# Optimization experiments

Hardware: AMD Instinct MI355X
Metric: run time of the kernel (lower is better)

## Reference

```python
import jax, jax.numpy as jnp
import numpy as np


def _conv(x, w, b, stride, pad):
    # NCHW conv, OIHW weights, bias add
    y = jax.lax.conv_general_dilated(
        x, w, (stride, stride), [(pad, pad), (pad, pad)],
        dimension_numbers=('NCHW', 'OIHW', 'NCHW'))
    return y + b[None, :, None, None]


def setup_inputs() -> dict:
    key = jax.random.key(0)
    ks = jax.random.split(key, 8)
    s = 0.05  # small init so SiLU chains stay numerically tame
    f32 = jnp.float32
    return {
        'x': jax.random.normal(ks[0], (8, 3, 640, 640), f32),
        'w0': jax.random.normal(ks[1], (32, 3, 3, 3), f32) * s,
        'b0': jnp.zeros((32,), f32),
        'w1': jax.random.normal(ks[2], (64, 32, 3, 3), f32) * s,
        'b1': jnp.zeros((64,), f32),
        'wc0': jax.random.normal(ks[3], (64, 64, 1, 1), f32) * s,
        'bc0': jnp.zeros((64,), f32),
        'wb1': jax.random.normal(ks[4], (32, 32, 3, 3), f32) * s,
        'bb1': jnp.zeros((32,), f32),
        'wb2': jax.random.normal(ks[5], (32, 32, 3, 3), f32) * s,
        'bb2': jnp.zeros((32,), f32),
        'wc1': jax.random.normal(ks[6], (64, 96, 1, 1), f32) * s,
        'bc1': jnp.zeros((64,), f32),
        'w3': jax.random.normal(ks[7], (128, 64, 3, 3), f32) * s,
        'b3': jnp.zeros((128,), f32),
    }


def reference(x, w0, b0, w1, b1, wc0, bc0, wb1, bb1, wb2, bb2, wc1, bc1, w3, b3):
    silu = jax.nn.silu
    # stem: conv0 (s2) + conv1 (s2), each Conv+SiLU
    h = silu(_conv(x, w0, b0, 2, 1))     # [B,32,320,320]
    h = silu(_conv(h, w1, b1, 2, 1))     # [B,64,160,160]
    # C2f block: 1x1 conv, split channels in half, residual bottleneck, concat, 1x1 conv
    y = silu(_conv(h, wc0, bc0, 1, 0))   # [B,64,160,160]
    x1, x2 = jnp.split(y, 2, axis=1)     # each [B,32,160,160]
    b = silu(_conv(x2, wb1, bb1, 1, 1))
    b = silu(_conv(b, wb2, bb2, 1, 1))
    b = x2 + b                           # shortcut=True bottleneck
    cat = jnp.concatenate([x1, x2, b], axis=1)  # [B,96,160,160] == 192*w
    h = silu(_conv(cat, wc1, bc1, 1, 0))  # [B,64,160,160]
    # conv3: downsample stage (s2)
    out = silu(_conv(h, w3, b3, 2, 1))    # [B,128,80,80]
    return out
```

## Files before the change

### kernel.cpp

```cpp
#include <hip/hip_runtime.h>
#include <hip/hip_bf16.h>

typedef __attribute__((ext_vector_type(8))) short short8;
typedef __attribute__((ext_vector_type(16))) float f32x16;
typedef __attribute__((ext_vector_type(4))) float f32x4;
typedef __attribute__((ext_vector_type(4))) unsigned int uint4v;
typedef __attribute__((ext_vector_type(4))) unsigned short ushort4v;

__device__ __forceinline__ float silu_f(float v) {
    return v * __builtin_amdgcn_rcpf(1.0f + __expf(-v));
}
__device__ __forceinline__ unsigned short bfhi(float v) {
    __hip_bfloat16 h = __float2bfloat16(v);
    return *reinterpret_cast<unsigned short*>(&h);
}
__device__ __forceinline__ float bf2f(unsigned short u) {
    __hip_bfloat16 h;
    *reinterpret_cast<unsigned short*>(&h) = u;
    return __bfloat162float(h);
}

__global__ __launch_bounds__(256) void prep_small(
    const float* __restrict__ w1, const float* __restrict__ wc0,
    const float* __restrict__ wb1, const float* __restrict__ wb2,
    const float* __restrict__ wc1, const float* __restrict__ w0,
    unsigned short* __restrict__ arena)
{
    const int u = blockIdx.x * 256 + threadIdx.x;
    if (u >= 6016) return;
    const int lane = u & 63, pf = u >> 6;
    float wv[8];
    if (pf < 36) {
        const int q = pf, cc = q & 1, rnd = (q >> 1) & 1, tap = q >> 2;
        const int co = cc * 32 + (lane & 31), ci0 = rnd * 16 + (lane >> 5) * 8;
        #pragma unroll
        for (int j = 0; j < 8; ++j) wv[j] = w1[(co * 32 + ci0 + j) * 9 + tap];
    } else if (pf < 44) {
        const int q = pf - 36, cc = q & 1, rnd = q >> 1;
        const int co = cc * 32 + (lane & 31), ci0 = rnd * 16 + (lane >> 5) * 8;
        #pragma unroll
        for (int j = 0; j < 8; ++j) wv[j] = wc0[co * 64 + ci0 + j];
    } else if (pf < 62) {
        const int q = pf - 44, rnd = q & 1, tap = q >> 1;
        const int co = lane & 31, ci0 = rnd * 16 + (lane >> 5) * 8;
        #pragma unroll
        for (int j = 0; j < 8; ++j) wv[j] = wb1[(co * 32 + ci0 + j) * 9 + tap];
    } else if (pf < 80) {
        const int q = pf - 62, rnd = q & 1, tap = q >> 1;
        const int co = lane & 31, ci0 = rnd * 16 + (lane >> 5) * 8;
        #pragma unroll
        for (int j = 0; j < 8; ++j) wv[j] = wb2[(co * 32 + ci0 + j) * 9 + tap];
    } else if (pf < 92) {
        const int q = pf - 80, cc = q & 1, rnd = q >> 1;
        const int co = cc * 32 + (lane & 31), ci0 = rnd * 16 + (lane >> 5) * 8;
        #pragma unroll
        for (int j = 0; j < 8; ++j) wv[j] = wc1[co * 96 + ci0 + j];
    } else {
        const int co = lane & 31;
        const int k0 = (pf - 92) * 16 + (lane >> 5) * 8;
        #pragma unroll
        for (int j = 0; j < 8; ++j) {
            const int k = k0 + j;
            wv[j] = (k < 27) ? w0[(co * 3 + k / 9) * 9 + (k % 9)] : 0.0f;
        }
    }
    unsigned short hs[8], ls[8];
    #pragma unroll
    for (int j = 0; j < 8; ++j) {
        unsigned short hh = bfhi(wv[j]);
        hs[j] = hh; ls[j] = bfhi(wv[j] - bf2f(hh));
    }
    *reinterpret_cast<short8*>(&arena[pf * 1024 + lane * 8])       = *(short8*)hs;
    *reinterpret_cast<short8*>(&arena[pf * 1024 + 512 + lane * 8]) = *(short8*)ls;
}

__global__ __launch_bounds__(256) void prep_w3(
    const float* __restrict__ w3, unsigned short* __restrict__ arena)
{
    const int u = blockIdx.x * 256 + threadIdx.x;
    const int lane = u & 63, pf = u >> 6;
    const int cc = pf & 1, rr = (pf >> 1) & 3, t9 = pf >> 3;
    const int tap = t9 % 9, cg = t9 / 9;
    const int co = cg * 64 + cc * 32 + (lane & 31);
    const int ci0 = rr * 16 + (lane >> 5) * 8;
    unsigned short hs[8], ls[8];
    #pragma unroll
    for (int j = 0; j < 8; ++j) {
        float wv = w3[(co * 64 + ci0 + j) * 9 + tap];
        unsigned short hh = bfhi(wv);
        hs[j] = hh; ls[j] = bfhi(wv - bf2f(hh));
    }
    *reinterpret_cast<short8*>(&arena[pf * 1024 + lane * 8])       = *(short8*)hs;
    *reinterpret_cast<short8*>(&arena[pf * 1024 + 512 + lane * 8]) = *(short8*)ls;
}

__global__ __launch_bounds__(256, 4) void stem_fused(
    const float* __restrict__ x, const unsigned short* __restrict__ wfr,
    const unsigned short* __restrict__ wc0fr, const float* __restrict__ b0,
    const float* __restrict__ bias, const float* __restrict__ bc0,
    unsigned short* __restrict__ ycl)
{
    __shared__ unsigned short lds[20800];
    const int tid = threadIdx.x;
    const int wv = tid >> 6, lane = tid & 63;
    const int p = lane & 31, h = lane >> 5;
    const int r = wv >> 1, cc = wv & 1;
    const int bx = blockIdx.x % 5, by = blockIdx.x / 5;
    const int ox0 = bx * 32, oy0 = by * 2;
    const int n = blockIdx.z;
    const float* xb = x + (long)n * 1228800;

    const int h8 = h * 8;
    int doff[16];
    #pragma unroll
    for (int idx = 0; idx < 16; ++idx) {
        const int k = (idx >> 3) * 16 + h8 + (idx & 7);
        if (k < 27) {
            const int ci = (k * 57) >> 9;
            const int tap = k - 9 * ci;
            const int dy = (tap * 11) >> 5, dx = tap - 3 * dy;
            doff[idx] = ci * 409600 + (dy - 1) * 640 + (dx - 1);
        } else {
            doff[idx] = 0;
        }
    }

    for (int it = 0; it < 3; ++it) {
        const int g = it * 4 + wv;
        if (g < 11) {
            const int rc = g * 32 + p;
            const bool validR = rc < 325;
            const int rec_c = validR ? rc : 324;
            int gp, row, col;
            if (rec_c < 64)       { gp = 0; row = rec_c >> 5; col = rec_c & 31; }
            else if (rec_c < 130) { gp = 1; int r2 = rec_c - 64;  row = r2 / 33; col = r2 - row * 33; }
            else if (rec_c < 226) { gp = 2; int r2 = rec_c - 130; row = r2 >> 5; col = r2 & 31; }
            else                  { gp = 3; int r2 = rec_c - 226; row = r2 / 33; col = r2 - row * 33; }
            const int gr = (gp >= 2) ? oy0 - 1 + row : oy0 + row;
            const int gc = (gp & 1)  ? ox0 - 1 + col : ox0 + col;
            const bool valid = validR && ((unsigned)gr < 160u) && ((unsigned)gc < 160u);
            const int Y = 2 * gr + (gp >> 1);
            const int X = 2 * gc + (gp & 1);
            const int Bsafe = valid ? (1280 * Y + 2 * X) : 641;
            const bool interior = valid && gr > 0 && gr < 159 && gc > 0 && gc < 159;
            const bool fastw = __all(interior);

            f32x16 a0;
            #pragma unroll
            for (int q = 0; q < 4; ++q) {
                f32x4 b4 = *reinterpret_cast<const f32x4*>(&b0[q * 8 + 4 * h]);
                #pragma unroll
                for (int r2 = 0; r2 < 4; ++r2) a0[q * 4 + r2] = b4[r2];
            }

            #pragma unroll
            for (int rnd = 0; rnd < 2; ++rnd) {
                unsigned short hs[8], ls[8];
                if (fastw) {
                    #pragma unroll
                    for (int j = 0; j < 8; ++j) {
                        float v = xb[Bsafe + doff[rnd * 8 + j]];
                        if (rnd == 1 && j >= 3) v = (h == 0) ? v : 0.0f;
                        unsigned short hh = bfhi(v);
                        hs[j] = hh; ls[j] = bfhi(v - bf2f(hh));
                    }
                } else {
                    #pragma unroll
                    for (int j = 0; j < 8; ++j) {
                        const int k = rnd * 16 + h8 + j;
                        const int ci = (k * 57) >> 9;
                        const int tap = k - 9 * ci;
                        const int dy = (tap * 11) >> 5, dx = tap - 3 * dy;
                        const int iy = 2 * Y + dy - 1;
                        const int ix = 2 * X + dx - 1;
                        bool ok = valid && ((unsigned)iy < 640u) && ((unsigned)ix < 640u);
                        if (rnd == 1 && j >= 3) ok = ok && (h == 0);
                        float v = ok ? xb[Bsafe + doff[rnd * 8 + j]] : 0.0f;
                        unsigned short hh = bfhi(v);
                        hs[j] = hh; ls[j] = bfhi(v - bf2f(hh));
                    }
                }
                short8 Bh = *(short8*)hs, Bl = *(short8*)ls;
                const unsigned short* fb = wfr + (92 + rnd) * 1024 + lane * 8;
                short8 Awh = *reinterpret_cast<const short8*>(fb);
                short8 Awl = *reinterpret_cast<const short8*>(fb + 512);
                a0 = __builtin_amdgcn_mfma_f32_32x32x16_bf16(Awh, Bh, a0, 0, 0, 0);
                a0 = __builtin_amdgcn_mfma_f32_32x32x16_bf16(Awh, Bl, a0, 0, 0, 0);
                a0 = __builtin_amdgcn_mfma_f32_32x32x16_bf16(Awl, Bh, a0, 0, 0, 0);
            }

            if (validR) {
                const int pm = rc & 7;
                #pragma unroll
                for (int q = 0; q < 4; ++q) {
                    ushort4v hv, lv;
                    #pragma unroll
                    for (int r2 = 0; r2 < 4; ++r2) {
                        float v = valid ? silu_f(a0[q * 4 + r2]) : 0.0f;
                        unsigned short hh = bfhi(v);
                        hv[r2] = hh; lv[r2] = bfhi(v - bf2f(hh));
                    }
                    *reinterpret_cast<ushort4v*>(&lds[rc * 64 + (((2 * q)     ^ pm) * 8) + 4 * h]) = hv;
                    *reinterpret_cast<ushort4v*>(&lds[rc * 64 + (((2 * q + 1) ^ pm) * 8) + 4 * h]) = lv;
                }
            }
        }
    }
    __syncthreads();

    f32x16 acc;
    #pragma unroll
    for (int q = 0; q < 4; ++q) {
        f32x4 b4 = *reinterpret_cast<const f32x4*>(&bias[cc * 32 + q * 8 + 4 * h]);
        #pragma unroll
        for (int r2 = 0; r2 < 4; ++r2) acc[q * 4 + r2] = b4[r2];
    }
    #pragma unroll
    for (int c = 0; c < 2; ++c) {
        #pragma unroll
        for (int tap = 0; tap < 9; ++tap) {
            const int dy = tap / 3 - 1, dx = tap % 3 - 1;
            const int ppy = dy & 1, ppx = dx & 1;
            const int toy = ppy ? ((dy == -1) ? 0 : 1) : 0;
            const int tox = ppx ? ((dx == -1) ? 0 : 1) : 0;
            const int gp = ppy * 2 + ppx;
            const int base = (gp == 0) ? 0 : (gp == 1) ? 64 : (gp == 2) ? 130 : 226;
            const int W = ppx ? 33 : 32;
            const int rec = base + (ppy ? (r + toy) : r) * W + (p + tox);
            const unsigned short* t = &lds[rec * 64];
            const int pm = rec & 7;
            short8 Bh = *reinterpret_cast<const short8*>(t + (((4 * c + 2 * h)     ^ pm) * 8));
            short8 Bl = *reinterpret_cast<const short8*>(t + (((4 * c + 2 * h + 1) ^ pm) * 8));
            const unsigned short* fb = wfr + ((tap * 2 + c) * 2 + cc) * 1024 + lane * 8;
            short8 Awh = *reinterpret_cast<const short8*>(fb);
            short8 Awl = *reinterpret_cast<const short8*>(fb + 512);
            acc = __builtin_amdgcn_mfma_f32_32x32x16_bf16(Awh, Bh, acc, 0, 0, 0);
            acc = __builtin_amdgcn_mfma_f32_32x32x16_bf16(Awh, Bl, acc, 0, 0, 0);
            acc = __builtin_amdgcn_mfma_f32_32x32x16_bf16(Awl, Bh, acc, 0, 0, 0);
        }
    }

    __syncthreads();
    {
        const int rec2 = r * 32 + p;
        #pragma unroll
        for (int q = 0; q < 4; ++q) {
            ushort4v hv, lv;
            #pragma unroll
            for (int r2 = 0; r2 < 4; ++r2) {
                float v = silu_f(acc[q * 4 + r2]);
                unsigned short hh = bfhi(v);
                hv[r2] = hh; lv[r2] = bfhi(v - bf2f(hh));
            }
            const int lsh = (2 * (cc * 4 + q))     ^ (rec2 & 15);
            const int lsl = (2 * (cc * 4 + q) + 1) ^ (rec2 & 15);
            *reinterpret_cast<ushort4v*>(&lds[rec2 * 128 + lsh * 8 + 4 * h]) = hv;
            *reinterpret_cast<ushort4v*>(&lds[rec2 * 128 + lsl * 8 + 4 * h]) = lv;
        }
    }
    __syncthreads();

    f32x16 a2;
    #pragma unroll
    for (int q = 0; q < 4; ++q) {
        f32x4 b4 = *reinterpret_cast<const f32x4*>(&bc0[cc * 32 + q * 8 + 4 * h]);
        #pragma unroll
        for (int r2 = 0; r2 < 4; ++r2) a2[q * 4 + r2] = b4[r2];
    }
    {
        const int rec2 = r * 32 + p;
        #pragma unroll
        for (int rnd = 0; rnd < 4; ++rnd) {
            const int sh = (4 * rnd + 2 * h)     ^ (rec2 & 15);
            const int sl = (4 * rnd + 2 * h + 1) ^ (rec2 & 15);
            short8 Bh = *reinterpret_cast<const short8*>(&lds[rec2 * 128 + sh * 8]);
            short8 Bl = *reinterpret_cast<const short8*>(&lds[rec2 * 128 + sl * 8]);
            const unsigned short* fb = wc0fr + (rnd * 2 + cc) * 1024 + lane * 8;
            short8 Awh = *reinterpret_cast<const short8*>(fb);
            short8 Awl = *reinterpret_cast<const short8*>(fb + 512);
            a2 = __builtin_amdgcn_mfma_f32_32x32x16_bf16(Awh, Bh, a2, 0, 0, 0);
            a2 = __builtin_amdgcn_mfma_f32_32x32x16_bf16(Awh, Bl, a2, 0, 0, 0);
            a2 = __builtin_amdgcn_mfma_f32_32x32x16_bf16(Awl, Bh, a2, 0, 0, 0);
        }
    }

    const int oy = oy0 + r;
    unsigned short* op = ycl + ((long)n * 25600 + (long)oy * 160 + ox0 + p) * 128;
    #pragma unroll
    for (int q = 0; q < 4; ++q) {
        ushort4v hv, lv;
        #pragma unroll
        for (int r2 = 0; r2 < 4; ++r2) {
            float v = silu_f(a2[q * 4 + r2]);
            unsigned short hh = bfhi(v);
            hv[r2] = hh; lv[r2] = bfhi(v - bf2f(hh));
        }
        const int gq = cc * 4 + q;
        *reinterpret_cast<ushort4v*>(op + gq * 16 + 4 * h)     = hv;
        *reinterpret_cast<ushort4v*>(op + gq * 16 + 8 + 4 * h) = lv;
    }
}

template <bool RESID>
__global__ __launch_bounds__(512, 4) void wb3x3(
    const unsigned short* __restrict__ in, int inRec, int inSlot0,
    const unsigned short* __restrict__ wfr, const float* __restrict__ bias,
    unsigned short* __restrict__ outb, const unsigned short* __restrict__ resid)
{
    __shared__ unsigned short lds[21760];
    const int tid = threadIdx.x;
    const int wv = tid >> 6, lane = tid & 63;
    const int p = lane & 31, h = lane >> 5;
    const int bx = blockIdx.x % 5, by = blockIdx.x / 5;
    const int ox0 = bx * 32, oy0 = by * 8;
    const int n = blockIdx.z;

    for (int u = tid; u < 2720; u += 512) {
        const int rec = u >> 3, s = u & 7;
        const int row = rec / 34, col = rec - row * 34;
        const int gr = oy0 - 1 + row, gc = ox0 - 1 + col;
        uint4v val = {0, 0, 0, 0};
        if (gr >= 0 && gr < 160 && gc >= 0 && gc < 160)
            val = *reinterpret_cast<const uint4v*>(
                in + ((long)n * 25600 + gr * 160 + gc) * inRec + (inSlot0 + s) * 8);
        *reinterpret_cast<uint4v*>(&lds[rec * 64 + ((s ^ (rec & 7)) * 8)]) = val;
    }

    f32x16 acc;
    #pragma unroll
    for (int q = 0; q < 4; ++q) {
        f32x4 b4 = *reinterpret_cast<const f32x4*>(&bias[q * 8 + 4 * h]);
        #pragma unroll
        for (int r = 0; r < 4; ++r) acc[q * 4 + r] = b4[r];
    }
    __syncthreads();

    #pragma unroll
    for (int tap = 0; tap < 9; ++tap) {
        const int dy = tap / 3 - 1, dx = tap % 3 - 1;
        const int rec = (wv + dy + 1) * 34 + (p + dx + 1);
        const unsigned short* t = &lds[rec * 64];
        short8 Bh[2], Bl[2];
        #pragma unroll
        for (int rnd = 0; rnd < 2; ++rnd) {
            Bh[rnd] = *reinterpret_cast<const short8*>(t + (((rnd*4 + 2*h)     ^ (rec & 7)) * 8));
            Bl[rnd] = *reinterpret_cast<const short8*>(t + (((rnd*4 + 2*h + 1) ^ (rec & 7)) * 8));
        }
        #pragma unroll
        for (int rnd = 0; rnd < 2; ++rnd) {
            const unsigned short* fb = wfr + (tap * 2 + rnd) * 1024 + lane * 8;
            short8 Awh = *reinterpret_cast<const short8*>(fb);
            short8 Awl = *reinterpret_cast<const short8*>(fb + 512);
            acc = __builtin_amdgcn_mfma_f32_32x32x16_bf16(Awh, Bh[rnd], acc, 0, 0, 0);
            acc = __builtin_amdgcn_mfma_f32_32x32x16_bf16(Awh, Bl[rnd], acc, 0, 0, 0);
            acc = __builtin_amdgcn_mfma_f32_32x32x16_bf16(Awl, Bh[rnd], acc, 0, 0, 0);
        }
    }

    const int oy = oy0 + wv;
    const long prow = (long)n * 25600 + (long)oy * 160 + ox0 + p;
    unsigned short* op = outb + prow * 64;
    const unsigned short* rp = RESID ? resid + prow * 128 : nullptr;
    #pragma unroll
    for (int q = 0; q < 4; ++q) {
        ushort4v hv, lv;
        float vs[4];
        #pragma unroll
        for (int r = 0; r < 4; ++r) vs[r] = silu_f(acc[q * 4 + r]);
        if (RESID) {
            ushort4v rh = *reinterpret_cast<const ushort4v*>(rp + (q + 4) * 16 + 4 * h);
            ushort4v rl = *reinterpret_cast<const ushort4v*>(rp + (q + 4) * 16 + 8 + 4 * h);
            #pragma unroll
            for (int r = 0; r < 4; ++r) vs[r] += bf2f(rh[r]) + bf2f(rl[r]);
        }
        #pragma unroll
        for (int r = 0; r < 4; ++r) {
            unsigned short hh = bfhi(vs[r]);
            hv[r] = hh; lv[r] = bfhi(vs[r] - bf2f(hh));
        }
        *reinterpret_cast<ushort4v*>(op + q * 16 + 4 * h)     = hv;
        *reinterpret_cast<ushort4v*>(op + q * 16 + 8 + 4 * h) = lv;
    }
}

template <int R1, int R2, bool POUT>
__global__ __launch_bounds__(512, 4) void wc1x1(
    const unsigned short* __restrict__ in1, int rec1,
    const unsigned short* __restrict__ in2, int rec2,
    const unsigned short* __restrict__ wfr, const float* __restrict__ bias,
    unsigned short* __restrict__ outb)
{
    constexpr int RT = R1 + R2;
    const int tid = threadIdx.x;
    const int wv = tid >> 6, lane = tid & 63;
    const int p = lane & 31, h = lane >> 5;
    const int n = blockIdx.z;
    const int px0 = blockIdx.x * 512;

    f32x16 acc[2][2];
    #pragma unroll
    for (int cc = 0; cc < 2; ++cc)
        #pragma unroll
        for (int q = 0; q < 4; ++q) {
            f32x4 b4 = *reinterpret_cast<const f32x4*>(&bias[cc * 32 + q * 8 + 4 * h]);
            #pragma unroll
            for (int r = 0; r < 4; ++r) { acc[cc][0][q*4+r] = b4[r]; acc[cc][1][q*4+r] = b4[r]; }
        }

    #pragma unroll
    for (int rnd = 0; rnd < RT; ++rnd) {
        const unsigned short* bp = (rnd < R1) ? in1 : in2;
        const int recN = (rnd < R1) ? rec1 : rec2;
        const int s0 = 4 * ((rnd < R1) ? rnd : rnd - R1);
        #pragma unroll
        for (int k = 0; k < 2; ++k) {
            const int px = px0 + (wv * 2 + k) * 32 + p;
            const unsigned short* sp = bp + ((long)n * 25600 + px) * recN + (s0 + 2 * h) * 8;
            short8 Bh = *reinterpret_cast<const short8*>(sp);
            short8 Bl = *reinterpret_cast<const short8*>(sp + 8);
            #pragma unroll
            for (int cc = 0; cc < 2; ++cc) {
                const unsigned short* fb = wfr + (rnd * 2 + cc) * 1024 + lane * 8;
                short8 Awh = *reinterpret_cast<const short8*>(fb);
                short8 Awl = *reinterpret_cast<const short8*>(fb + 512);
                acc[cc][k] = __builtin_amdgcn_mfma_f32_32x32x16_bf16(Awh, Bh, acc[cc][k], 0, 0, 0);
                acc[cc][k] = __builtin_amdgcn_mfma_f32_32x32x16_bf16(Awh, Bl, acc[cc][k], 0, 0, 0);
                acc[cc][k] = __builtin_amdgcn_mfma_f32_32x32x16_bf16(Awl, Bh, acc[cc][k], 0, 0, 0);
            }
        }
    }

    #pragma unroll
    for (int k = 0; k < 2; ++k) {
        const int px = px0 + (wv * 2 + k) * 32 + p;
        unsigned short* op;
        if (POUT) {
            const int y = px / 160, xx = px % 160;
            const int pl = (y & 1) * 2 + (xx & 1);
            op = outb + (((long)n * 4 + pl) * 6400 + (y >> 1) * 80 + (xx >> 1)) * 128;
        } else {
            op = outb + ((long)n * 25600 + px) * 128;
        }
        #pragma unroll
        for (int cc = 0; cc < 2; ++cc)
            #pragma unroll
            for (int q = 0; q < 4; ++q) {
                ushort4v hv, lv;
                #pragma unroll
                for (int r = 0; r < 4; ++r) {
                    float v = silu_f(acc[cc][k][q * 4 + r]);
                    unsigned short hh = bfhi(v);
                    hv[r] = hh; lv[r] = bfhi(v - bf2f(hh));
                }
                const int gq = cc * 4 + q;
                *reinterpret_cast<ushort4v*>(op + gq * 16 + 4 * h)     = hv;
                *reinterpret_cast<ushort4v*>(op + gq * 16 + 8 + 4 * h) = lv;
            }
    }
}

__global__ __launch_bounds__(512, 4) void conv3_one(
    const unsigned short* __restrict__ h2p, const unsigned short* __restrict__ wfr,
    const float* __restrict__ bias, float* __restrict__ outf)
{
    __shared__ unsigned short lds[34848];
    const int tid = threadIdx.x;
    const int wv = tid >> 6, lane = tid & 63;
    const int p = lane & 31, h = lane >> 5;
    const int bx = blockIdx.x % 5, by = blockIdx.x / 5;
    const int ox0 = bx * 16, oy0 = by * 16;
    const int cg = blockIdx.y;
    const int co0 = cg * 64;
    const int n = blockIdx.z;

    f32x16 acc[2];
    #pragma unroll
    for (int cc = 0; cc < 2; ++cc)
        #pragma unroll
        for (int q = 0; q < 4; ++q) {
            f32x4 b4 = *reinterpret_cast<const f32x4*>(&bias[co0 + cc * 32 + q * 8 + 4 * h]);
            #pragma unroll
            for (int r = 0; r < 4; ++r) acc[cc][q * 4 + r] = b4[r];
        }

    for (int rr = 0; rr < 4; ++rr) {
        __syncthreads();
        for (int u = tid; u < 4356; u += 512) {
            const int rec = u >> 2, s = u & 3;
            int gp, row, col;
            if (rec < 256)      { gp = 0; row = rec >> 4; col = rec & 15; }
            else if (rec < 528) { gp = 1; int r2 = rec - 256; row = r2 / 17; col = r2 - row * 17; }
            else if (rec < 800) { gp = 2; int r2 = rec - 528; row = r2 >> 4; col = r2 & 15; }
            else                { gp = 3; int r2 = rec - 800; row = r2 / 17; col = r2 - row * 17; }
            const int gr = (gp >= 2) ? oy0 - 1 + row : oy0 + row;
            const int gc = (gp & 1)  ? ox0 - 1 + col : ox0 + col;
            uint4v val = {0, 0, 0, 0};
            if (gr >= 0 && gr < 80 && gc >= 0 && gc < 80)
                val = *reinterpret_cast<const uint4v*>(
                    h2p + (((long)n * 4 + gp) * 6400 + gr * 80 + gc) * 128 + (rr * 4 + s) * 8);
            *reinterpret_cast<uint4v*>(&lds[rec * 32 + ((s ^ ((rec >> 1) & 3)) * 8)]) = val;
        }
        __syncthreads();

        #pragma unroll
        for (int tap = 0; tap < 9; ++tap) {
            const int dy = tap / 3 - 1, dx = tap % 3 - 1;
            const int ppy = dy & 1, ppx = dx & 1;
            const int toy = ppy ? ((dy == -1) ? 0 : 1) : 0;
            const int tox = ppx ? ((dx == -1) ? 0 : 1) : 0;
            const int gp = ppy * 2 + ppx;
            const int base = (gp == 0) ? 0 : (gp == 1) ? 256 : (gp == 2) ? 528 : 800;
            const int W = ppx ? 17 : 16;
            const int rl = wv * 2 + (p >> 4), cl = p & 15;
            const int rec = base + (ppy ? (rl + toy) : rl) * W + (cl + tox);
            const unsigned short* t = &lds[rec * 32];
            const int pm = (rec >> 1) & 3;
            short8 Bh = *reinterpret_cast<const short8*>(t + (((2*h)     ^ pm) * 8));
            short8 Bl = *reinterpret_cast<const short8*>(t + (((2*h + 1) ^ pm) * 8));
            #pragma unroll
            for (int cc = 0; cc < 2; ++cc) {
                const unsigned short* fb =
                    wfr + (((cg * 9 + tap) * 4 + rr) * 2 + cc) * 1024 + lane * 8;
                short8 Awh = *reinterpret_cast<const short8*>(fb);
                short8 Awl = *reinterpret_cast<const short8*>(fb + 512);
                acc[cc] = __builtin_amdgcn_mfma_f32_32x32x16_bf16(Awh, Bh, acc[cc], 0, 0, 0);
                acc[cc] = __builtin_amdgcn_mfma_f32_32x32x16_bf16(Awh, Bl, acc[cc], 0, 0, 0);
                acc[cc] = __builtin_amdgcn_mfma_f32_32x32x16_bf16(Awl, Bh, acc[cc], 0, 0, 0);
            }
        }
    }

    const int rl = wv * 2 + (p >> 4);
    const int oy = oy0 + rl;
    const int pxg = oy * 80 + ox0 + (p & 15);
    #pragma unroll
    for (int cc = 0; cc < 2; ++cc)
        #pragma unroll
        for (int q = 0; q < 4; ++q)
            #pragma unroll
            for (int r = 0; r < 4; ++r) {
                const int co = co0 + cc * 32 + q * 8 + 4 * h + r;
                outf[((long)n * 128 + co) * 6400 + pxg] = silu_f(acc[cc][q * 4 + r]);
            }
}

extern "C" void kernel_launch(void* const* d_in, const int* in_sizes, int n_in,
                              void* d_out, int out_size, void* d_ws, size_t ws_size,
                              hipStream_t stream) {
    const float* x   = (const float*)d_in[0];
    const float* w0  = (const float*)d_in[1];
    const float* b0  = (const float*)d_in[2];
    const float* w1  = (const float*)d_in[3];
    const float* b1  = (const float*)d_in[4];
    const float* wc0 = (const float*)d_in[5];
    const float* bc0 = (const float*)d_in[6];
    const float* wb1 = (const float*)d_in[7];
    const float* bb1 = (const float*)d_in[8];
    const float* wb2 = (const float*)d_in[9];
    const float* bb2 = (const float*)d_in[10];
    const float* wc1 = (const float*)d_in[11];
    const float* bc1 = (const float*)d_in[12];
    const float* w3  = (const float*)d_in[13];
    const float* b3  = (const float*)d_in[14];

    unsigned short* u = (unsigned short*)d_ws;
    unsigned short* ycl  = u + 52428800L;
    unsigned short* b1cl = u + 26214400L;
    unsigned short* bcl  = u + 39321600L;
    unsigned short* h2p  = u;
    unsigned short* w3a  = u + 26214400L;

    unsigned short* wsa = (unsigned short*)d_out;
    unsigned short* a_conv1 = wsa;
    unsigned short* a_wc0   = wsa + 36 * 1024;
    unsigned short* a_wb1   = wsa + 44 * 1024;
    unsigned short* a_wb2   = wsa + 62 * 1024;
    unsigned short* a_wc1   = wsa + 80 * 1024;

    prep_small<<<dim3(24, 1, 1), dim3(256, 1, 1), 0, stream>>>(
        w1, wc0, wb1, wb2, wc1, w0, wsa);

    stem_fused<<<dim3(400, 1, 8), dim3(256, 1, 1), 0, stream>>>(
        x, a_conv1, a_wc0, b0, b1, bc0, ycl);

    wb3x3<false><<<dim3(100, 1, 8), dim3(512, 1, 1), 0, stream>>>(
        ycl, 128, 8, a_wb1, bb1, b1cl, nullptr);

    wb3x3<true><<<dim3(100, 1, 8), dim3(512, 1, 1), 0, stream>>>(
        b1cl, 64, 0, a_wb2, bb2, bcl, ycl);

    prep_w3<<<dim3(36, 1, 1), dim3(256, 1, 1), 0, stream>>>(w3, w3a);

    wc1x1<4, 2, true><<<dim3(50, 1, 8), dim3(512, 1, 1), 0, stream>>>(
        ycl, 128, bcl, 64, a_wc1, bc1, h2p);

    conv3_one<<<dim3(25, 2, 8), dim3(512, 1, 1), 0, stream>>>(h2p, w3a, b3, (float*)d_out);
}
```

Before: 246.2 us.

## Halve LDS tiles in 3x3 convs by staging channels in smaller chunks

The bottleneck 3x3 kernel now stages its input tile in two half-channel passes, and the stride-2 conv3 kernel stages the high and low bf16 split parts in separate passes. This halves shared memory per block, so more blocks can be resident per CU under the 4-block launch bound. The cost is extra __syncthreads barriers and extra reload rounds that reduce overlap inside each block, plus a branch on the pass index in conv3's inner loop.

```diff
diff --git a/kernel.cpp b/kernel.cpp
--- a/kernel.cpp
+++ b/kernel.cpp
@@ -307,7 +307,7 @@
     const unsigned short* __restrict__ wfr, const float* __restrict__ bias,
     unsigned short* __restrict__ outb, const unsigned short* __restrict__ resid)
 {
-    __shared__ unsigned short lds[21760];
+    __shared__ unsigned short lds[10880];
     const int tid = threadIdx.x;
     const int wv = tid >> 6, lane = tid & 63;
     const int p = lane & 31, h = lane >> 5;
@@ -315,17 +315,6 @@
     const int ox0 = bx * 32, oy0 = by * 8;
     const int n = blockIdx.z;
 
-    for (int u = tid; u < 2720; u += 512) {
-        const int rec = u >> 3, s = u & 7;
-        const int row = rec / 34, col = rec - row * 34;
-        const int gr = oy0 - 1 + row, gc = ox0 - 1 + col;
-        uint4v val = {0, 0, 0, 0};
-        if (gr >= 0 && gr < 160 && gc >= 0 && gc < 160)
-            val = *reinterpret_cast<const uint4v*>(
-                in + ((long)n * 25600 + gr * 160 + gc) * inRec + (inSlot0 + s) * 8);
-        *reinterpret_cast<uint4v*>(&lds[rec * 64 + ((s ^ (rec & 7)) * 8)]) = val;
-    }
-
     f32x16 acc;
     #pragma unroll
     for (int q = 0; q < 4; ++q) {
@@ -333,27 +322,34 @@
         #pragma unroll
         for (int r = 0; r < 4; ++r) acc[q * 4 + r] = b4[r];
     }
-    __syncthreads();
-
-    #pragma unroll
-    for (int tap = 0; tap < 9; ++tap) {
-        const int dy = tap / 3 - 1, dx = tap % 3 - 1;
-        const int rec = (wv + dy + 1) * 34 + (p + dx + 1);
-        const unsigned short* t = &lds[rec * 64];
-        short8 Bh[2], Bl[2];
-        #pragma unroll
-        for (int rnd = 0; rnd < 2; ++rnd) {
-            Bh[rnd] = *reinterpret_cast<const short8*>(t + (((rnd*4 + 2*h)     ^ (rec & 7)) * 8));
-            Bl[rnd] = *reinterpret_cast<const short8*>(t + (((rnd*4 + 2*h + 1) ^ (rec & 7)) * 8));
-        }
-        #pragma unroll
-        for (int rnd = 0; rnd < 2; ++rnd) {
-            const unsigned short* fb = wfr + (tap * 2 + rnd) * 1024 + lane * 8;
+
+    for (int c = 0; c < 2; ++c) {
+        __syncthreads();
+        for (int u = tid; u < 1360; u += 512) {
+            const int rec = u >> 2, s = u & 3;
+            const int row = rec / 34, col = rec - row * 34;
+            const int gr = oy0 - 1 + row, gc = ox0 - 1 + col;
+            uint4v val = {0, 0, 0, 0};
+            if (gr >= 0 && gr < 160 && gc >= 0 && gc < 160)
+                val = *reinterpret_cast<const uint4v*>(
+                    in + ((long)n * 25600 + gr * 160 + gc) * inRec + (inSlot0 + 4 * c + s) * 8);
+            *reinterpret_cast<uint4v*>(&lds[rec * 32 + ((s ^ (rec & 3)) * 8)]) = val;
+        }
+        __syncthreads();
+
+        #pragma unroll
+        for (int tap = 0; tap < 9; ++tap) {
+            const int dy = tap / 3 - 1, dx = tap % 3 - 1;
+            const int rec = (wv + dy + 1) * 34 + (p + dx + 1);
+            const unsigned short* t = &lds[rec * 32];
+            short8 Bh = *reinterpret_cast<const short8*>(t + (((2 * h)     ^ (rec & 3)) * 8));
+            short8 Bl = *reinterpret_cast<const short8*>(t + (((2 * h + 1) ^ (rec & 3)) * 8));
+            const unsigned short* fb = wfr + (tap * 2 + c) * 1024 + lane * 8;
             short8 Awh = *reinterpret_cast<const short8*>(fb);
             short8 Awl = *reinterpret_cast<const short8*>(fb + 512);
-            acc = __builtin_amdgcn_mfma_f32_32x32x16_bf16(Awh, Bh[rnd], acc, 0, 0, 0);
-            acc = __builtin_amdgcn_mfma_f32_32x32x16_bf16(Awh, Bl[rnd], acc, 0, 0, 0);
-            acc = __builtin_amdgcn_mfma_f32_32x32x16_bf16(Awl, Bh[rnd], acc, 0, 0, 0);
+            acc = __builtin_amdgcn_mfma_f32_32x32x16_bf16(Awh, Bh, acc, 0, 0, 0);
+            acc = __builtin_amdgcn_mfma_f32_32x32x16_bf16(Awh, Bl, acc, 0, 0, 0);
+            acc = __builtin_amdgcn_mfma_f32_32x32x16_bf16(Awl, Bh, acc, 0, 0, 0);
         }
     }
 
@@ -463,7 +459,7 @@
     const unsigned short* __restrict__ h2p, const unsigned short* __restrict__ wfr,
     const float* __restrict__ bias, float* __restrict__ outf)
 {
-    __shared__ unsigned short lds[34848];
+    __shared__ unsigned short lds[17424];
     const int tid = threadIdx.x;
     const int wv = tid >> 6, lane = tid & 63;
     const int p = lane & 31, h = lane >> 5;
@@ -483,10 +479,11 @@
             for (int r = 0; r < 4; ++r) acc[cc][q * 4 + r] = b4[r];
         }
 
-    for (int rr = 0; rr < 4; ++rr) {
+    for (int r8 = 0; r8 < 8; ++r8) {
+        const int rr = r8 >> 1, k = r8 & 1;
         __syncthreads();
-        for (int u = tid; u < 4356; u += 512) {
-            const int rec = u >> 2, s = u & 3;
+        for (int u = tid; u < 2178; u += 512) {
+            const int rec = u >> 1, s = u & 1;
             int gp, row, col;
             if (rec < 256)      { gp = 0; row = rec >> 4; col = rec & 15; }
             else if (rec < 528) { gp = 1; int r2 = rec - 256; row = r2 / 17; col = r2 - row * 17; }
@@ -497,8 +494,8 @@
             uint4v val = {0, 0, 0, 0};
             if (gr >= 0 && gr < 80 && gc >= 0 && gc < 80)
                 val = *reinterpret_cast<const uint4v*>(
-                    h2p + (((long)n * 4 + gp) * 6400 + gr * 80 + gc) * 128 + (rr * 4 + s) * 8);
-            *reinterpret_cast<uint4v*>(&lds[rec * 32 + ((s ^ ((rec >> 1) & 3)) * 8)]) = val;
+                    h2p + (((long)n * 4 + gp) * 6400 + gr * 80 + gc) * 128 + (rr * 4 + 2 * s + k) * 8);
+            *reinterpret_cast<uint4v*>(&lds[rec * 16 + ((s ^ (rec & 1)) * 8)]) = val;
         }
         __syncthreads();
 
@@ -513,19 +510,20 @@
             const int W = ppx ? 17 : 16;
             const int rl = wv * 2 + (p >> 4), cl = p & 15;
             const int rec = base + (ppy ? (rl + toy) : rl) * W + (cl + tox);
-            const unsigned short* t = &lds[rec * 32];
-            const int pm = (rec >> 1) & 3;
-            short8 Bh = *reinterpret_cast<const short8*>(t + (((2*h)     ^ pm) * 8));
-            short8 Bl = *reinterpret_cast<const short8*>(t + (((2*h + 1) ^ pm) * 8));
+            short8 Bq = *reinterpret_cast<const short8*>(
+                &lds[rec * 16 + ((h ^ (rec & 1)) * 8)]);
             #pragma unroll
             for (int cc = 0; cc < 2; ++cc) {
                 const unsigned short* fb =
                     wfr + (((cg * 9 + tap) * 4 + rr) * 2 + cc) * 1024 + lane * 8;
                 short8 Awh = *reinterpret_cast<const short8*>(fb);
-                short8 Awl = *reinterpret_cast<const short8*>(fb + 512);
-                acc[cc] = __builtin_amdgcn_mfma_f32_32x32x16_bf16(Awh, Bh, acc[cc], 0, 0, 0);
-                acc[cc] = __builtin_amdgcn_mfma_f32_32x32x16_bf16(Awh, Bl, acc[cc], 0, 0, 0);
-                acc[cc] = __builtin_amdgcn_mfma_f32_32x32x16_bf16(Awl, Bh, acc[cc], 0, 0, 0);
+                if (k == 0) {
+                    short8 Awl = *reinterpret_cast<const short8*>(fb + 512);
+                    acc[cc] = __builtin_amdgcn_mfma_f32_32x32x16_bf16(Awh, Bq, acc[cc], 0, 0, 0);
+                    acc[cc] = __builtin_amdgcn_mfma_f32_32x32x16_bf16(Awl, Bq, acc[cc], 0, 0, 0);
+                } else {
+                    acc[cc] = __builtin_amdgcn_mfma_f32_32x32x16_bf16(Awh, Bq, acc[cc], 0, 0, 0);
+                }
             }
         }
     }
```

Result: slower. 286.4 us (+16.3%).
